# Optimization experiments

Measured on AMD Instinct MI355X. Metric: run time of the kernel, lower is better.

## Reference

```python
import jax, jax.numpy as jnp
import numpy as np

EMBED_DIM = 1024
NUM_HEADS = 16
HEAD_DIM = EMBED_DIM // NUM_HEADS
BATCH = 2
SEQ = 2048


def setup_inputs() -> dict:
    key = jax.random.key(0)
    k_x, k_wi, k_bi, k_wo, k_bo = jax.random.split(key, 5)
    scale_in = 1.0 / np.sqrt(EMBED_DIM)
    x = jax.random.normal(k_x, (BATCH, SEQ, EMBED_DIM), dtype=jnp.float32)
    # nn.Linear stores weight [out, in]; we keep [in, out] for x @ W.
    w_in = jax.random.uniform(k_wi, (EMBED_DIM, 3 * EMBED_DIM), jnp.float32, -scale_in, scale_in)
    b_in = jax.random.uniform(k_bi, (3 * EMBED_DIM,), jnp.float32, -scale_in, scale_in)
    w_out = jax.random.uniform(k_wo, (EMBED_DIM, EMBED_DIM), jnp.float32, -scale_in, scale_in)
    b_out = jax.random.uniform(k_bo, (EMBED_DIM,), jnp.float32, -scale_in, scale_in)
    return {"x": x, "w_in": w_in, "b_in": b_in, "w_out": w_out, "b_out": b_out}


def reference(x, w_in, b_in, w_out, b_out):
    B, S, E = x.shape
    H, D = NUM_HEADS, HEAD_DIM
    inp = x @ w_in + b_in                       # [B,S,3E]
    que, key, val = jnp.split(inp, 3, axis=-1)  # each [B,S,E]
    que = que.reshape(B, S, H, D)
    key = key.reshape(B, S, H, D)
    val = val.reshape(B, S, H, D)
    scores = jnp.einsum('bshd,brhd->bhsr', que, key) * (1.0 / np.sqrt(D))
    weights = jax.nn.softmax(scores, axis=-1)   # [B,H,S,S]
    attn = jnp.einsum('bhsr,brhd->bshd', weights, val).reshape(B, S, E)
    return attn @ w_out + b_out
```

## Files before the change

### kernel.cpp

```cpp
#include <hip/hip_runtime.h>


typedef __bf16 bf16x8 __attribute__((ext_vector_type(8)));
typedef float  f32x4  __attribute__((ext_vector_type(4)));
typedef short  s16x4  __attribute__((ext_vector_type(4)));
typedef short  s16x8  __attribute__((ext_vector_type(8)));

__device__ __forceinline__ unsigned short f2b(float f) {
  unsigned u = __float_as_uint(f);
  unsigned r = u + 0x7fffu + ((u >> 16) & 1u);
  return (unsigned short)(r >> 16);
}

__device__ __forceinline__ unsigned cvt_pk_bf16(float a, float b) {
#if defined(__HIP_DEVICE_COMPILE__)
  unsigned r;
  asm("v_cvt_pk_bf16_f32 %0, %1, %2" : "=v"(r) : "v"(a), "v"(b));
  return r;
#else
  return (unsigned)f2b(a) | ((unsigned)f2b(b) << 16);
#endif
}

__device__ __forceinline__ void gl_lds16(const void* g, void* l) {
  __builtin_amdgcn_global_load_lds(
      (__attribute__((address_space(1))) void*)g,
      (__attribute__((address_space(3))) void*)l, 16, 0, 0);
}

__device__ __forceinline__ f32x4 mfma16x16x16(s16x4 a, s16x4 b, f32x4 c) {
#if defined(__HIP_DEVICE_COMPILE__)
#if __has_builtin(__builtin_amdgcn_mfma_f32_16x16x16bf16_1k)
  return __builtin_amdgcn_mfma_f32_16x16x16bf16_1k(a, b, c, 0, 0, 0);
#else
  s16x8 a8 = {a[0], a[1], a[2], a[3], 0, 0, 0, 0};
  s16x8 b8 = {b[0], b[1], b[2], b[3], 0, 0, 0, 0};
  union U { s16x8 s; bf16x8 v; };
  U ua, ub; ua.s = a8; ub.s = b8;
  return __builtin_amdgcn_mfma_f32_16x16x32_bf16(ua.v, ub.v, c, 0, 0, 0);
#endif
#else
  (void)a; (void)b;
  return c;
#endif
}

__global__ __launch_bounds__(256) void cast_kernel(
    const float* __restrict__ in, unsigned short* __restrict__ out, int n4) {
  int i = blockIdx.x * 256 + threadIdx.x;
  if (i < n4) {
    float4 v = ((const float4*)in)[i];
    ushort4 o;
    o.x = f2b(v.x); o.y = f2b(v.y); o.z = f2b(v.z); o.w = f2b(v.w);
    ((ushort4*)out)[i] = o;
  }
}

__global__ __launch_bounds__(256) void transpose_cast_kernel(
    const float* __restrict__ in, unsigned short* __restrict__ out, int R, int C) {
  __shared__ float tile[64][65];
  int r0 = blockIdx.y * 64, c0 = blockIdx.x * 64;
  int tid = threadIdx.x;
#pragma unroll
  for (int p = 0; p < 16; p++) {
    int i = tid + p * 256;
    int ri = i >> 6, ci = i & 63;
    tile[ri][ci] = in[(size_t)(r0 + ri) * C + c0 + ci];
  }
  __syncthreads();
#pragma unroll
  for (int p = 0; p < 16; p++) {
    int i = tid + p * 256;
    int ci = i >> 6, ri = i & 63;
    out[(size_t)(c0 + ci) * R + r0 + ri] = f2b(tile[ri][ci]);
  }
}

__global__ __launch_bounds__(256) void vt_transpose_kernel(
    const unsigned short* __restrict__ qkv, unsigned short* __restrict__ vt) {
  __shared__ unsigned short tile[64][65];
  int bid = blockIdx.x;
  int st = bid & 31, h = (bid >> 5) & 15, b = bid >> 9;
  int s0 = st * 64;
  int tid = threadIdx.x;
  const unsigned short* src = qkv + (size_t)(b * 2048 + s0) * 3072 + 2048 + h * 64;
#pragma unroll
  for (int p = 0; p < 16; p++) {
    int i = tid + p * 256;
    int sr = i >> 6, d = i & 63;
    tile[sr][d] = src[(size_t)sr * 3072 + d];
  }
  __syncthreads();
  unsigned short* dst = vt + (size_t)(b * 16 + h) * 64 * 2048 + s0;
#pragma unroll
  for (int p = 0; p < 16; p++) {
    int i = tid + p * 256;
    int dr = i >> 6, sc = i & 63;
    dst[(size_t)dr * 2048 + sc] = tile[sc][dr];
  }
}

template <int OUT_BF16>
__global__ __launch_bounds__(256) void gemm_bt(
    const unsigned short* __restrict__ A, const unsigned short* __restrict__ Bt,
    const float* __restrict__ bias, void* __restrict__ Cp, int M, int N, int K,
    int qcols, float qscale) {
  __shared__ __align__(16) unsigned short As[128 * 32];
  __shared__ __align__(16) unsigned short Bs[128 * 32];
  int tid = threadIdx.x;
  int wave = tid >> 6, lane = tid & 63;
  int m_l = lane & 15, quad = lane >> 4;
  int wm = (wave >> 1) * 64, wn = (wave & 1) * 64;
  int row = tid >> 2, kp = (tid & 3) << 3;
  const unsigned short* ag = A + (size_t)(blockIdx.y * 128 + row) * K + kp;
  const unsigned short* bg = Bt + (size_t)(blockIdx.x * 128 + row) * K + kp;
  unsigned short* asw = As + wave * 512;
  unsigned short* bsw = Bs + wave * 512;
  f32x4 acc[4][4] = {};
  for (int k0 = 0; k0 < K; k0 += 32) {
    __syncthreads();
    gl_lds16(ag + k0, asw);
    gl_lds16(ag + (size_t)64 * K + k0, asw + 2048);
    gl_lds16(bg + k0, bsw);
    gl_lds16(bg + (size_t)64 * K + k0, bsw + 2048);
    __syncthreads();
    bf16x8 af[4], bf[4];
#pragma unroll
    for (int i = 0; i < 4; i++)
      af[i] = *(const bf16x8*)&As[(wm + i * 16 + m_l) * 32 + quad * 8];
#pragma unroll
    for (int j = 0; j < 4; j++)
      bf[j] = *(const bf16x8*)&Bs[(wn + j * 16 + m_l) * 32 + quad * 8];
#pragma unroll
    for (int i = 0; i < 4; i++)
#pragma unroll
      for (int j = 0; j < 4; j++)
        acc[i][j] = __builtin_amdgcn_mfma_f32_16x16x32_bf16(af[i], bf[j], acc[i][j], 0, 0, 0);
  }
  float bv[4];
#pragma unroll
  for (int j = 0; j < 4; j++) bv[j] = bias[blockIdx.x * 128 + wn + j * 16 + m_l];
#pragma unroll
  for (int i = 0; i < 4; i++) {
    int m = blockIdx.y * 128 + wm + i * 16 + quad * 4;
#pragma unroll
    for (int j = 0; j < 4; j++) {
      int n = blockIdx.x * 128 + wn + j * 16 + m_l;
      float sc = (OUT_BF16 && n < qcols) ? qscale : 1.0f;
#pragma unroll
      for (int r = 0; r < 4; r++) {
        float v = (acc[i][j][r] + bv[j]) * sc;
        if (OUT_BF16)
          ((unsigned short*)Cp)[(size_t)(m + r) * N + n] = f2b(v);
        else
          ((float*)Cp)[(size_t)(m + r) * N + n] = v;
      }
    }
  }
}

__global__ __launch_bounds__(512) void attn_kernel(
    const unsigned short* __restrict__ qkv, const unsigned short* __restrict__ vt,
    unsigned short* __restrict__ aout) {
  __shared__ __align__(16) unsigned short Qs[128 * 64];
  __shared__ __align__(16) unsigned short Ks[64 * 64];
  __shared__ __align__(16) unsigned short Vts[64 * 64];
  int bid = blockIdx.x;
  int qt = bid & 15, h = (bid >> 4) & 15, b = bid >> 8;
  int tid = threadIdx.x, wave = tid >> 6;
  int lane = tid & 63;
  int m_l = lane & 15, quad = lane >> 4;
  int q0 = qt * 128;
  const unsigned short* qb = qkv + (size_t)b * 2048 * 3072 + h * 64;
  const unsigned short* kb = qb + 1024;
  const unsigned short* vtb = vt + (size_t)(b * 16 + h) * 64 * 2048;

  int srow = tid >> 3;
  int sd0 = ((tid & 7) ^ (srow & 7)) * 8;

  gl_lds16(qb + (size_t)(q0 + srow) * 3072 + sd0, Qs + wave * 512);
  gl_lds16(qb + (size_t)(q0 + 64 + srow) * 3072 + sd0, Qs + 4096 + wave * 512);
  __syncthreads();

  int sw0 = ((quad ^ (m_l & 7)) * 8);
  int sw1 = (((quad + 4) ^ (m_l & 7)) * 8);

  int qrow = (wave * 16 + m_l) * 64;
  bf16x8 qf0 = *(const bf16x8*)&Qs[qrow + sw0];
  bf16x8 qf1 = *(const bf16x8*)&Qs[qrow + sw1];

  f32x4 o[4] = {};
  float lp = 0.f;

  for (int kt = 0; kt < 2048; kt += 64) {
    __syncthreads();
    gl_lds16(kb + (size_t)(kt + srow) * 3072 + sd0, Ks + wave * 512);
    gl_lds16(vtb + (size_t)srow * 2048 + kt + sd0, Vts + wave * 512);
    __syncthreads();

#pragma unroll
    for (int t = 0; t < 4; t++) {
      int kr = (t * 16 + m_l) * 64;
      bf16x8 kf0 = *(const bf16x8*)&Ks[kr + sw0];
      bf16x8 kf1 = *(const bf16x8*)&Ks[kr + sw1];
      f32x4 z = {};
      f32x4 s = __builtin_amdgcn_mfma_f32_16x16x32_bf16(kf0, qf0, z, 0, 0, 0);
      s = __builtin_amdgcn_mfma_f32_16x16x32_bf16(kf1, qf1, s, 0, 0, 0);
      float p0 = __builtin_exp2f(s[0]);
      float p1 = __builtin_exp2f(s[1]);
      float p2 = __builtin_exp2f(s[2]);
      float p3 = __builtin_exp2f(s[3]);
      lp += (p0 + p1) + (p2 + p3);
      union { uint2 u; s16x4 s4; } pk;
      pk.u.x = cvt_pk_bf16(p0, p1);
      pk.u.y = cvt_pk_bf16(p2, p3);
#pragma unroll
      for (int dt = 0; dt < 4; dt++) {
        int drow = dt * 16 + m_l;
        int kchunk = (t * 2 + (quad >> 1)) ^ (m_l & 7);
        s16x4 vf = *(const s16x4*)&Vts[drow * 64 + kchunk * 8 + (quad & 1) * 4];
        o[dt] = mfma16x16x16(vf, pk.s4, o[dt]);
      }
    }
  }

  lp += __shfl_xor(lp, 16, 64);
  lp += __shfl_xor(lp, 32, 64);
  float rl = 1.0f / lp;

  unsigned short* ob = aout + (size_t)(b * 2048 + q0 + wave * 16 + m_l) * 1024 +
                       h * 64 + quad * 4;
#pragma unroll
  for (int dt = 0; dt < 4; dt++) {
    union { uint2 u; ushort4 w; } pk;
    pk.u.x = cvt_pk_bf16(o[dt][0] * rl, o[dt][1] * rl);
    pk.u.y = cvt_pk_bf16(o[dt][2] * rl, o[dt][3] * rl);
    *(ushort4*)&ob[dt * 16] = pk.w;
  }
}

extern "C" void kernel_launch(void* const* d_in, const int* in_sizes, int n_in,
                              void* d_out, int out_size, void* d_ws, size_t ws_size,
                              hipStream_t stream) {
  (void)in_sizes; (void)n_in; (void)out_size; (void)ws_size;
  const float* x     = (const float*)d_in[0];
  const float* w_in  = (const float*)d_in[1];
  const float* b_in  = (const float*)d_in[2];
  const float* w_out = (const float*)d_in[3];
  const float* b_out = (const float*)d_in[4];
  char* ws = (char*)d_ws;
  unsigned short* xb    = (unsigned short*)(ws + 0);
  unsigned short* wint  = (unsigned short*)(ws + 8388608);
  unsigned short* woutt = (unsigned short*)(ws + 14680064);
  unsigned short* qkv   = (unsigned short*)(ws + 16777216);
  unsigned short* vt    = (unsigned short*)(ws + 41943040);
  unsigned short* attn  = (unsigned short*)(ws + 50331648);
  float* out = (float*)d_out;

  const float QSCALE = 0.125f * 1.44269504088896f;

  cast_kernel<<<4096, 256, 0, stream>>>(x, xb, 1048576);
  transpose_cast_kernel<<<dim3(48, 16), 256, 0, stream>>>(w_in, wint, 1024, 3072);
  transpose_cast_kernel<<<dim3(16, 16), 256, 0, stream>>>(w_out, woutt, 1024, 1024);
  gemm_bt<1><<<dim3(24, 32), 256, 0, stream>>>(xb, wint, b_in, qkv, 4096, 3072, 1024,
                                               1024, QSCALE);
  vt_transpose_kernel<<<1024, 256, 0, stream>>>(qkv, vt);
  attn_kernel<<<512, 512, 0, stream>>>(qkv, vt, attn);
  gemm_bt<0><<<dim3(8, 32), 256, 0, stream>>>(attn, woutt, b_out, out, 4096, 1024, 1024,
                                              0, 1.0f);
}
```

Measured before the change: 215.0 us.

## Split attention into 64-query blocks and compute row sums via MFMA

```diff
diff --git a/kernel.cpp b/kernel.cpp
--- a/kernel.cpp
+++ b/kernel.cpp
@@ -159,18 +159,18 @@
   }
 }
 
-__global__ __launch_bounds__(512) void attn_kernel(
+__global__ __launch_bounds__(256) void attn_kernel(
     const unsigned short* __restrict__ qkv, const unsigned short* __restrict__ vt,
     unsigned short* __restrict__ aout) {
-  __shared__ __align__(16) unsigned short Qs[128 * 64];
+  __shared__ __align__(16) unsigned short Qs[64 * 64];
   __shared__ __align__(16) unsigned short Ks[64 * 64];
   __shared__ __align__(16) unsigned short Vts[64 * 64];
   int bid = blockIdx.x;
-  int qt = bid & 15, h = (bid >> 4) & 15, b = bid >> 8;
+  int qt = bid & 31, h = (bid >> 5) & 15, b = bid >> 9;
   int tid = threadIdx.x, wave = tid >> 6;
   int lane = tid & 63;
   int m_l = lane & 15, quad = lane >> 4;
-  int q0 = qt * 128;
+  int q0 = qt * 64;
   const unsigned short* qb = qkv + (size_t)b * 2048 * 3072 + h * 64;
   const unsigned short* kb = qb + 1024;
   const unsigned short* vtb = vt + (size_t)(b * 16 + h) * 64 * 2048;
@@ -179,54 +179,55 @@
   int sd0 = ((tid & 7) ^ (srow & 7)) * 8;
 
   gl_lds16(qb + (size_t)(q0 + srow) * 3072 + sd0, Qs + wave * 512);
-  gl_lds16(qb + (size_t)(q0 + 64 + srow) * 3072 + sd0, Qs + 4096 + wave * 512);
+  gl_lds16(qb + (size_t)(q0 + 32 + srow) * 3072 + sd0, Qs + 2048 + wave * 512);
   __syncthreads();
 
-  int sw0 = ((quad ^ (m_l & 7)) * 8);
-  int sw1 = (((quad + 4) ^ (m_l & 7)) * 8);
+  int ml7 = m_l & 7;
+  int sw0 = ((quad ^ ml7) * 8);
+  int sw1 = (((quad + 4) ^ ml7) * 8);
 
   int qrow = (wave * 16 + m_l) * 64;
   bf16x8 qf0 = *(const bf16x8*)&Qs[qrow + sw0];
   bf16x8 qf1 = *(const bf16x8*)&Qs[qrow + sw1];
 
+  int kbase = m_l * 64;
+  int vbase = m_l * 64 + (quad & 1) * 4;
+  int qh = quad >> 1;
+
+  const s16x4 ones = {0x3F80, 0x3F80, 0x3F80, 0x3F80};
+
   f32x4 o[4] = {};
-  float lp = 0.f;
+  f32x4 lacc = {};
 
   for (int kt = 0; kt < 2048; kt += 64) {
     __syncthreads();
     gl_lds16(kb + (size_t)(kt + srow) * 3072 + sd0, Ks + wave * 512);
+    gl_lds16(kb + (size_t)(kt + 32 + srow) * 3072 + sd0, Ks + 2048 + wave * 512);
     gl_lds16(vtb + (size_t)srow * 2048 + kt + sd0, Vts + wave * 512);
+    gl_lds16(vtb + (size_t)(32 + srow) * 2048 + kt + sd0, Vts + 2048 + wave * 512);
     __syncthreads();
 
 #pragma unroll
     for (int t = 0; t < 4; t++) {
-      int kr = (t * 16 + m_l) * 64;
-      bf16x8 kf0 = *(const bf16x8*)&Ks[kr + sw0];
-      bf16x8 kf1 = *(const bf16x8*)&Ks[kr + sw1];
+      bf16x8 kf0 = *(const bf16x8*)&Ks[kbase + t * 1024 + sw0];
+      bf16x8 kf1 = *(const bf16x8*)&Ks[kbase + t * 1024 + sw1];
       f32x4 z = {};
       f32x4 s = __builtin_amdgcn_mfma_f32_16x16x32_bf16(kf0, qf0, z, 0, 0, 0);
       s = __builtin_amdgcn_mfma_f32_16x16x32_bf16(kf1, qf1, s, 0, 0, 0);
-      float p0 = __builtin_exp2f(s[0]);
-      float p1 = __builtin_exp2f(s[1]);
-      float p2 = __builtin_exp2f(s[2]);
-      float p3 = __builtin_exp2f(s[3]);
-      lp += (p0 + p1) + (p2 + p3);
       union { uint2 u; s16x4 s4; } pk;
-      pk.u.x = cvt_pk_bf16(p0, p1);
-      pk.u.y = cvt_pk_bf16(p2, p3);
+      pk.u.x = cvt_pk_bf16(__builtin_exp2f(s[0]), __builtin_exp2f(s[1]));
+      pk.u.y = cvt_pk_bf16(__builtin_exp2f(s[2]), __builtin_exp2f(s[3]));
+      lacc = mfma16x16x16(ones, pk.s4, lacc);
+      int voff = vbase + (((t * 2 + qh) ^ ml7) * 8);
 #pragma unroll
       for (int dt = 0; dt < 4; dt++) {
-        int drow = dt * 16 + m_l;
-        int kchunk = (t * 2 + (quad >> 1)) ^ (m_l & 7);
-        s16x4 vf = *(const s16x4*)&Vts[drow * 64 + kchunk * 8 + (quad & 1) * 4];
+        s16x4 vf = *(const s16x4*)&Vts[voff + dt * 1024];
         o[dt] = mfma16x16x16(vf, pk.s4, o[dt]);
       }
     }
   }
 
-  lp += __shfl_xor(lp, 16, 64);
-  lp += __shfl_xor(lp, 32, 64);
-  float rl = 1.0f / lp;
+  float rl = 1.0f / lacc[0];
 
   unsigned short* ob = aout + (size_t)(b * 2048 + q0 + wave * 16 + m_l) * 1024 +
                        h * 64 + quad * 4;
@@ -265,7 +266,7 @@
   gemm_bt<1><<<dim3(24, 32), 256, 0, stream>>>(xb, wint, b_in, qkv, 4096, 3072, 1024,
                                                1024, QSCALE);
   vt_transpose_kernel<<<1024, 256, 0, stream>>>(qkv, vt);
-  attn_kernel<<<512, 512, 0, stream>>>(qkv, vt, attn);
+  attn_kernel<<<1024, 256, 0, stream>>>(qkv, vt, attn);
   gemm_bt<0><<<dim3(8, 32), 256, 0, stream>>>(attn, woutt, b_out, out, 4096, 1024, 1024,
                                               0, 1.0f);
 }
```

Result: slower. 224.1 us (+4.3%).
